# Kernel tuning notes

Hardware: AMD Instinct MI355X
Metric: run time of the kernel (lower is better)

Reference implementation:

```python
import jax, jax.numpy as jnp
import numpy as np

B, L, D = 4, 2048, 512
H = 8
DK = 512 // H  # 64
DV = 512 // H  # 64
TEMP = float(np.power(DK, 0.5))
LN_EPS = 1e-5


def setup_inputs() -> dict:
    key = jax.random.key(0)
    ks = jax.random.split(key, 12)
    s = 0.02
    return {
        "q": jax.random.normal(ks[0], (B, L, D), jnp.float32),
        "k": jax.random.normal(ks[1], (B, L, D), jnp.float32),
        "v": jax.random.normal(ks[2], (B, L, D), jnp.float32),
        "mask": jax.random.randint(ks[3], (B, L, L), 0, 2, jnp.int32),
        "wq_w": jax.random.normal(ks[4], (H * DK, D), jnp.float32) * s,
        "wq_b": jnp.zeros((H * DK,), jnp.float32),
        "wv_w": jax.random.normal(ks[5], (H * DV, D), jnp.float32) * s,
        "wv_b": jnp.zeros((H * DV,), jnp.float32),
        "fc_w": jax.random.normal(ks[6], (D, H * DV), jnp.float32) * s,
        "fc_b": jnp.zeros((D,), jnp.float32),
        "ln_g": jnp.ones((D,), jnp.float32),
        "ln_b": jnp.zeros((D,), jnp.float32),
    }


def reference(q, k, v, mask, wq_w, wq_b, wv_w, wv_b, fc_w, fc_b, ln_g, ln_b):
    residual = q
    # NOTE: source module projects k with w_qs (bug preserved faithfully)
    qh = (q @ wq_w.T + wq_b).reshape(B, L, H, DK).transpose(0, 2, 1, 3)  # bhld
    kh = (k @ wq_w.T + wq_b).reshape(B, L, H, DK).transpose(0, 2, 1, 3)
    vh = (v @ wv_w.T + wv_b).reshape(B, L, H, DV).transpose(0, 2, 1, 3)
    attn = jnp.einsum("bhqd,bhkd->bhqk", qh / TEMP, kh)
    attn = jnp.where(mask[:, None, :, :] == 1, -1e9, attn)
    attn = jax.nn.softmax(attn, axis=-1)
    out = jnp.einsum("bhqk,bhkd->bhqd", attn, vh)  # (B, H, L, DV)
    # faithful buffer reinterpretation: .view(n_head, sz_b, L, DV)
    out = out.reshape(H, B, L, DV).transpose(0, 2, 1, 3).reshape(B, L, H * DV)
    out = out @ fc_w.T + fc_b
    x = out + residual
    mu = jnp.mean(x, axis=-1, keepdims=True)
    var = jnp.mean(jnp.square(x - mu), axis=-1, keepdims=True)
    y = (x - mu) / jnp.sqrt(var + LN_EPS) * ln_g + ln_b
    return (y, attn)
```

## Files before the change

### kernel.cpp

```cpp
#include <hip/hip_runtime.h>

#define NB 4
#define NL 2048
#define ND 512
#define NH 8
#define NTOK (NB * NL)

constexpr float LN_EPS = 1e-5f;

typedef __attribute__((ext_vector_type(8))) short bf16x8;
typedef __attribute__((ext_vector_type(4))) float f32x4;

static __device__ __forceinline__ unsigned short f2bf(float f) {
  unsigned u = __builtin_bit_cast(unsigned, f);
  unsigned r = (u + 0x7fffu + ((u >> 16) & 1u)) >> 16;
  return (unsigned short)r;
}

#define GEMM_CORE(X, W)                                                        \
  __shared__ float As[16][64];                                                 \
  __shared__ float Bs[16][64];                                                 \
  const int tid = threadIdx.x;                                                 \
  const int tx = tid & 15, ty = tid >> 4;                                      \
  const int m0 = blockIdx.x * 64, n0 = blockIdx.y * 64;                        \
  const int lrow = tid >> 2, lseg = tid & 3;                                   \
  float acc[4][4] = {};                                                        \
  for (int k0 = 0; k0 < 512; k0 += 16) {                                       \
    const float4 xa = *(const float4*)&X[(size_t)(m0 + lrow) * ND + k0 + lseg * 4]; \
    const float4 wb = *(const float4*)&W[(size_t)(n0 + lrow) * ND + k0 + lseg * 4]; \
    __syncthreads();                                                           \
    As[lseg * 4 + 0][lrow] = xa.x;                                             \
    As[lseg * 4 + 1][lrow] = xa.y;                                             \
    As[lseg * 4 + 2][lrow] = xa.z;                                             \
    As[lseg * 4 + 3][lrow] = xa.w;                                             \
    Bs[lseg * 4 + 0][lrow] = wb.x;                                             \
    Bs[lseg * 4 + 1][lrow] = wb.y;                                             \
    Bs[lseg * 4 + 2][lrow] = wb.z;                                             \
    Bs[lseg * 4 + 3][lrow] = wb.w;                                             \
    __syncthreads();                                                           \
    _Pragma("unroll") for (int kk = 0; kk < 16; ++kk) {                        \
      float av[4], bv[4];                                                      \
      {                                                                        \
        const float4 t = *(const float4*)&As[kk][ty * 4];                      \
        av[0] = t.x; av[1] = t.y; av[2] = t.z; av[3] = t.w;                    \
      }                                                                        \
      {                                                                        \
        const float4 t = *(const float4*)&Bs[kk][tx * 4];                      \
        bv[0] = t.x; bv[1] = t.y; bv[2] = t.z; bv[3] = t.w;                    \
      }                                                                        \
      _Pragma("unroll") for (int i = 0; i < 4; ++i)                            \
      _Pragma("unroll") for (int j = 0; j < 4; ++j)                            \
        acc[i][j] += av[i] * bv[j];                                            \
    }                                                                          \
  }

__global__ __launch_bounds__(256) void gemm_qk_bf16(const float* __restrict__ X,
                                                    const float* __restrict__ W,
                                                    const float* __restrict__ bias,
                                                    unsigned short* __restrict__ out,
                                                    float scale) {
  GEMM_CORE(X, W)
  const int oc = n0 + tx * 4;
  const int hh = n0 >> 6;
#pragma unroll
  for (int i = 0; i < 4; ++i) {
    const int n = m0 + ty * 4 + i;
    const int bb = n >> 11, l = n & 2047;
    ushort4 o;
    o.x = f2bf((acc[i][0] + bias[oc + 0]) * scale);
    o.y = f2bf((acc[i][1] + bias[oc + 1]) * scale);
    o.z = f2bf((acc[i][2] + bias[oc + 2]) * scale);
    o.w = f2bf((acc[i][3] + bias[oc + 3]) * scale);
    *(ushort4*)&out[(((size_t)bb * NH + hh) * NL + l) * 64 + tx * 4] = o;
  }
}

__global__ __launch_bounds__(256) void gemm_v_bf16t(const float* __restrict__ X,
                                                    const float* __restrict__ W,
                                                    const float* __restrict__ bias,
                                                    unsigned short* __restrict__ outT) {
  GEMM_CORE(X, W)
  const int oc = n0 + tx * 4;
  const int hh = n0 >> 6;
  const int n_base = m0 + ty * 4;
  const int bb = n_base >> 11;
  const int l0 = n_base & 2047;
#pragma unroll
  for (int j = 0; j < 4; ++j) {
    const int d = tx * 4 + j;
    ushort4 o;
    o.x = f2bf(acc[0][j] + bias[oc + j]);
    o.y = f2bf(acc[1][j] + bias[oc + j]);
    o.z = f2bf(acc[2][j] + bias[oc + j]);
    o.w = f2bf(acc[3][j] + bias[oc + j]);
    *(ushort4*)&outT[(((size_t)bb * NH + hh) * 64 + d) * NL + l0] = o;
  }
}

__global__ __launch_bounds__(256) void attn_mfma(const unsigned short* __restrict__ qh,
                                                 const unsigned short* __restrict__ kh,
                                                 const unsigned short* __restrict__ vT,
                                                 const int* __restrict__ mask,
                                                 float* __restrict__ attn,
                                                 float* __restrict__ ao) {
  const int b = blockIdx.z, h = blockIdx.y, q0 = blockIdx.x * 64;
  const int bh = b * NH + h;
  __shared__ unsigned short Ks[64 * 72];
  __shared__ unsigned short Vt[64 * 72];
  __shared__ unsigned short Ps[4 * 16 * 72];
  const int tid = threadIdx.x;
  const int w = tid >> 6, lane = tid & 63;
  const int quad = lane >> 4, l15 = lane & 15;

  const size_t qoff = ((size_t)bh * NL + q0 + w * 16 + l15) * 64 + quad * 8;
  const bf16x8 aq0 = *(const bf16x8*)(qh + qoff);
  const bf16x8 aq1 = *(const bf16x8*)(qh + qoff + 32);

  const int srow = tid >> 2;
  const int scol = (tid & 3) * 16;

  float rinv[4] = {0.f, 0.f, 0.f, 0.f};
  unsigned int mbits[16];
#pragma unroll
  for (int i = 0; i < 16; ++i) mbits[i] = 0;

  for (int kt = 0; kt < 32; ++kt) {
    const unsigned short* kg = kh + ((size_t)bh * NL + kt * 64 + srow) * 64 + scol;
    const uint4 k0 = *(const uint4*)kg;
    const uint4 k1 = *(const uint4*)(kg + 8);
    __syncthreads();
    *(uint4*)&Ks[srow * 72 + scol] = k0;
    *(uint4*)&Ks[srow * 72 + scol + 8] = k1;
    __syncthreads();
    f32x4 s[4];
#pragma unroll
    for (int nt = 0; nt < 4; ++nt) {
      const bf16x8 b0 = *(const bf16x8*)&Ks[(nt * 16 + l15) * 72 + quad * 8];
      const bf16x8 b1 = *(const bf16x8*)&Ks[(nt * 16 + l15) * 72 + 32 + quad * 8];
      f32x4 acc = {0.f, 0.f, 0.f, 0.f};
      acc = __builtin_amdgcn_mfma_f32_16x16x32_bf16(aq0, b0, acc, 0, 0, 0);
      acc = __builtin_amdgcn_mfma_f32_16x16x32_bf16(aq1, b1, acc, 0, 0, 0);
      s[nt] = acc;
    }
    unsigned int mb = 0;
#pragma unroll
    for (int r = 0; r < 4; ++r) {
      const size_t mrow = ((size_t)b * NL + q0 + w * 16 + quad * 4 + r) * NL + kt * 64;
#pragma unroll
      for (int nt = 0; nt < 4; ++nt) {
        const int mz = mask[mrow + nt * 16 + l15];
        float e = __expf(s[nt][r]);
        if (mz == 1) {
          mb |= (1u << (nt * 4 + r));
          e = 0.f;
        }
        rinv[r] += e;
      }
    }
    mbits[kt >> 1] |= mb << ((kt & 1) * 16);
  }
#pragma unroll
  for (int r = 0; r < 4; ++r) {
    float v = rinv[r];
    v += __shfl_xor(v, 1);
    v += __shfl_xor(v, 2);
    v += __shfl_xor(v, 4);
    v += __shfl_xor(v, 8);
    rinv[r] = 1.0f / v;
  }

  f32x4 oacc[4];
#pragma unroll
  for (int nt = 0; nt < 4; ++nt) oacc[nt] = (f32x4){0.f, 0.f, 0.f, 0.f};

  for (int kt = 0; kt < 32; ++kt) {
    const unsigned short* kg = kh + ((size_t)bh * NL + kt * 64 + srow) * 64 + scol;
    const unsigned short* vg = vT + ((size_t)bh * 64 + srow) * NL + kt * 64 + scol;
    const uint4 k0 = *(const uint4*)kg;
    const uint4 k1 = *(const uint4*)(kg + 8);
    const uint4 v0 = *(const uint4*)vg;
    const uint4 v1 = *(const uint4*)(vg + 8);
    __syncthreads();
    *(uint4*)&Ks[srow * 72 + scol] = k0;
    *(uint4*)&Ks[srow * 72 + scol + 8] = k1;
    *(uint4*)&Vt[srow * 72 + scol] = v0;
    *(uint4*)&Vt[srow * 72 + scol + 8] = v1;
    __syncthreads();
    f32x4 s[4];
#pragma unroll
    for (int nt = 0; nt < 4; ++nt) {
      const bf16x8 b0 = *(const bf16x8*)&Ks[(nt * 16 + l15) * 72 + quad * 8];
      const bf16x8 b1 = *(const bf16x8*)&Ks[(nt * 16 + l15) * 72 + 32 + quad * 8];
      f32x4 acc = {0.f, 0.f, 0.f, 0.f};
      acc = __builtin_amdgcn_mfma_f32_16x16x32_bf16(aq0, b0, acc, 0, 0, 0);
      acc = __builtin_amdgcn_mfma_f32_16x16x32_bf16(aq1, b1, acc, 0, 0, 0);
      s[nt] = acc;
    }
    const unsigned int mb = mbits[kt >> 1] >> ((kt & 1) * 16);
#pragma unroll
    for (int r = 0; r < 4; ++r) {
      const int q = q0 + w * 16 + quad * 4 + r;
      float* arow = attn + ((size_t)bh * NL + q) * NL + kt * 64;
      unsigned short* prow = &Ps[(w * 16 + quad * 4 + r) * 72];
#pragma unroll
      for (int nt = 0; nt < 4; ++nt) {
        float e = ((mb >> (nt * 4 + r)) & 1u) ? 0.f : __expf(s[nt][r]) * rinv[r];
        arow[nt * 16 + l15] = e;
        prow[nt * 16 + l15] = f2bf(e);
      }
    }
    const bf16x8 pa0 = *(const bf16x8*)&Ps[(w * 16 + l15) * 72 + quad * 8];
    const bf16x8 pa1 = *(const bf16x8*)&Ps[(w * 16 + l15) * 72 + 32 + quad * 8];
#pragma unroll
    for (int nt = 0; nt < 4; ++nt) {
      const bf16x8 vb0 = *(const bf16x8*)&Vt[(nt * 16 + l15) * 72 + quad * 8];
      const bf16x8 vb1 = *(const bf16x8*)&Vt[(nt * 16 + l15) * 72 + 32 + quad * 8];
      oacc[nt] = __builtin_amdgcn_mfma_f32_16x16x32_bf16(pa0, vb0, oacc[nt], 0, 0, 0);
      oacc[nt] = __builtin_amdgcn_mfma_f32_16x16x32_bf16(pa1, vb1, oacc[nt], 0, 0, 0);
    }
  }
#pragma unroll
  for (int r = 0; r < 4; ++r) {
    float* orow = ao + ((size_t)bh * NL + q0 + w * 16 + quad * 4 + r) * 64;
#pragma unroll
    for (int nt = 0; nt < 4; ++nt) orow[nt * 16 + l15] = oacc[nt][r];
  }
}

__global__ __launch_bounds__(256) void fc_gather(const float* __restrict__ AO,
                                                 const float* __restrict__ W,
                                                 const float* __restrict__ bias,
                                                 const float* __restrict__ resid,
                                                 float* __restrict__ Xout) {
  __shared__ float As[16][64];
  __shared__ float Bs[16][64];
  const int tid = threadIdx.x;
  const int tx = tid & 15, ty = tid >> 4;
  const int m0 = blockIdx.x * 64, n0 = blockIdx.y * 64;
  const int lrow = tid >> 2, lseg = tid & 3;
  const int n = m0 + lrow;
  const int b_out = n >> 11;
  const int l_out = n & 2047;
  const int h2 = b_out * 2 + (l_out >> 10);
  const int q2base = (l_out & 1023) << 1;
  float acc[4][4] = {};
  for (int k0 = 0; k0 < 512; k0 += 16) {
    const int c = k0 + lseg * 4;
    const int q2 = q2base | ((c >> 8) & 1);
    const int b2 = (c >> 6) & 3;
    const int d2 = c & 63;
    const float4 xa = *(const float4*)&AO[((size_t)(h2 * 4 + b2) * NL + q2) * 64 + d2];
    const float4 wb = *(const float4*)&W[(size_t)(n0 + lrow) * ND + c];
    __syncthreads();
    As[lseg * 4 + 0][lrow] = xa.x;
    As[lseg * 4 + 1][lrow] = xa.y;
    As[lseg * 4 + 2][lrow] = xa.z;
    As[lseg * 4 + 3][lrow] = xa.w;
    Bs[lseg * 4 + 0][lrow] = wb.x;
    Bs[lseg * 4 + 1][lrow] = wb.y;
    Bs[lseg * 4 + 2][lrow] = wb.z;
    Bs[lseg * 4 + 3][lrow] = wb.w;
    __syncthreads();
#pragma unroll
    for (int kk = 0; kk < 16; ++kk) {
      float av[4], bv[4];
      {
        const float4 t = *(const float4*)&As[kk][ty * 4];
        av[0] = t.x; av[1] = t.y; av[2] = t.z; av[3] = t.w;
      }
      {
        const float4 t = *(const float4*)&Bs[kk][tx * 4];
        bv[0] = t.x; bv[1] = t.y; bv[2] = t.z; bv[3] = t.w;
      }
#pragma unroll
      for (int i = 0; i < 4; ++i)
#pragma unroll
        for (int j = 0; j < 4; ++j) acc[i][j] += av[i] * bv[j];
    }
  }
  const int oc = n0 + tx * 4;
#pragma unroll
  for (int i = 0; i < 4; ++i) {
    const float4 r = *(const float4*)&resid[(size_t)(m0 + ty * 4 + i) * ND + oc];
    float4 o;
    o.x = acc[i][0] + bias[oc + 0] + r.x;
    o.y = acc[i][1] + bias[oc + 1] + r.y;
    o.z = acc[i][2] + bias[oc + 2] + r.z;
    o.w = acc[i][3] + bias[oc + 3] + r.w;
    *(float4*)&Xout[(size_t)(m0 + ty * 4 + i) * ND + oc] = o;
  }
}

__global__ __launch_bounds__(64) void layernorm_k(const float* __restrict__ x,
                                                  const float* __restrict__ g,
                                                  const float* __restrict__ bta,
                                                  float* __restrict__ y) {
  const int n = blockIdx.x;
  const int lane = threadIdx.x;
  const float* row = x + (size_t)n * ND;
  const float4 a = *(const float4*)&row[lane * 8];
  const float4 c = *(const float4*)&row[lane * 8 + 4];
  float s = a.x + a.y + a.z + a.w + c.x + c.y + c.z + c.w;
  float sq = a.x * a.x + a.y * a.y + a.z * a.z + a.w * a.w +
             c.x * c.x + c.y * c.y + c.z * c.z + c.w * c.w;
#pragma unroll
  for (int off = 32; off; off >>= 1) {
    s += __shfl_down(s, off);
    sq += __shfl_down(sq, off);
  }
  s = __shfl(s, 0);
  sq = __shfl(sq, 0);
  const float mu = s * (1.f / 512.f);
  const float var = sq * (1.f / 512.f) - mu * mu;
  const float rstd = rsqrtf(var + LN_EPS);
  float* yo = y + (size_t)n * ND;
  const int c0 = lane * 8;
  float4 o1, o2;
  o1.x = (a.x - mu) * rstd * g[c0 + 0] + bta[c0 + 0];
  o1.y = (a.y - mu) * rstd * g[c0 + 1] + bta[c0 + 1];
  o1.z = (a.z - mu) * rstd * g[c0 + 2] + bta[c0 + 2];
  o1.w = (a.w - mu) * rstd * g[c0 + 3] + bta[c0 + 3];
  o2.x = (c.x - mu) * rstd * g[c0 + 4] + bta[c0 + 4];
  o2.y = (c.y - mu) * rstd * g[c0 + 5] + bta[c0 + 5];
  o2.z = (c.z - mu) * rstd * g[c0 + 6] + bta[c0 + 6];
  o2.w = (c.w - mu) * rstd * g[c0 + 7] + bta[c0 + 7];
  *(float4*)&yo[c0] = o1;
  *(float4*)&yo[c0 + 4] = o2;
}

extern "C" void kernel_launch(void* const* d_in, const int* in_sizes, int n_in,
                              void* d_out, int out_size, void* d_ws, size_t ws_size,
                              hipStream_t stream) {
  const float* q = (const float*)d_in[0];
  const float* k = (const float*)d_in[1];
  const float* v = (const float*)d_in[2];
  const int* mask = (const int*)d_in[3];
  const float* wq_w = (const float*)d_in[4];
  const float* wq_b = (const float*)d_in[5];
  const float* wv_w = (const float*)d_in[6];
  const float* wv_b = (const float*)d_in[7];
  const float* fc_w = (const float*)d_in[8];
  const float* fc_b = (const float*)d_in[9];
  const float* ln_g = (const float*)d_in[10];
  const float* ln_b = (const float*)d_in[11];

  float* y = (float*)d_out;
  float* attn = y + (size_t)NTOK * ND;

  const size_t SZ = (size_t)NTOK * ND;
  unsigned short* qhb = (unsigned short*)d_ws;
  unsigned short* khb = qhb + SZ;
  unsigned short* vTb = khb + SZ;
  float* ao = (float*)(vTb + SZ);
  float* xx = ao + SZ;

  const dim3 gproj(NTOK / 64, ND / 64);
  gemm_qk_bf16<<<gproj, 256, 0, stream>>>(q, wq_w, wq_b, qhb, 0.125f);
  gemm_qk_bf16<<<gproj, 256, 0, stream>>>(k, wq_w, wq_b, khb, 1.0f);
  gemm_v_bf16t<<<gproj, 256, 0, stream>>>(v, wv_w, wv_b, vTb);
  attn_mfma<<<dim3(NL / 64, NH, NB), 256, 0, stream>>>(qhb, khb, vTb, mask, attn, ao);
  fc_gather<<<gproj, 256, 0, stream>>>(ao, fc_w, fc_b, q, xx);
  layernorm_k<<<NTOK, 64, 0, stream>>>(xx, ln_g, ln_b, y);
}
```

Baseline: 0.9995 ms.

## Replace fp32 SIMT projection and output GEMMs with bf16 MFMA kernels

The Q/K/V projection GEMMs and the gathered output-projection GEMM now convert fp32 tiles to bf16 in shared memory and use 16x16x32 bf16 MFMA instructions instead of scalar fp32 FMAs. Each k-step now covers 64 elements instead of 16. The Q/K and transposed-V outputs are staged through shared memory so global stores are coalesced and wide. The aim is to cut the compute cost of the dense projections, at the price of bf16 rounding of the inputs, including the fc input that was previously kept in fp32.

```diff
diff --git a/kernel.cpp b/kernel.cpp
--- a/kernel.cpp
+++ b/kernel.cpp
@@ -17,84 +17,104 @@
   return (unsigned short)r;
 }
 
-#define GEMM_CORE(X, W)                                                        \
-  __shared__ float As[16][64];                                                 \
-  __shared__ float Bs[16][64];                                                 \
+static __device__ __forceinline__ uint2 pk4(const float4 f) {
+  uint2 r;
+  r.x = (unsigned)f2bf(f.x) | ((unsigned)f2bf(f.y) << 16);
+  r.y = (unsigned)f2bf(f.z) | ((unsigned)f2bf(f.w) << 16);
+  return r;
+}
+
+#define MFMA_GEMM_PRELUDE                                                      \
+  __shared__ unsigned short As[64 * 72];                                       \
+  __shared__ unsigned short Bs[64 * 72];                                       \
   const int tid = threadIdx.x;                                                 \
-  const int tx = tid & 15, ty = tid >> 4;                                      \
+  const int w = tid >> 6;                                                      \
+  const int lane = tid & 63;                                                   \
+  const int quad = lane >> 4, l15 = lane & 15;                                 \
   const int m0 = blockIdx.x * 64, n0 = blockIdx.y * 64;                        \
-  const int lrow = tid >> 2, lseg = tid & 3;                                   \
-  float acc[4][4] = {};                                                        \
-  for (int k0 = 0; k0 < 512; k0 += 16) {                                       \
-    const float4 xa = *(const float4*)&X[(size_t)(m0 + lrow) * ND + k0 + lseg * 4]; \
-    const float4 wb = *(const float4*)&W[(size_t)(n0 + lrow) * ND + k0 + lseg * 4]; \
+  const int srow = tid >> 2;                                                   \
+  const int c4 = (tid & 3) * 4;                                                \
+  const int scol = (tid & 3) * 16;                                             \
+  f32x4 acc[4];                                                                \
+  acc[0] = acc[1] = acc[2] = acc[3] = (f32x4){0.f, 0.f, 0.f, 0.f};
+
+#define MFMA_STEP(AV, BV)                                                      \
+  do {                                                                         \
     __syncthreads();                                                           \
-    As[lseg * 4 + 0][lrow] = xa.x;                                             \
-    As[lseg * 4 + 1][lrow] = xa.y;                                             \
-    As[lseg * 4 + 2][lrow] = xa.z;                                             \
-    As[lseg * 4 + 3][lrow] = xa.w;                                             \
-    Bs[lseg * 4 + 0][lrow] = wb.x;                                             \
-    Bs[lseg * 4 + 1][lrow] = wb.y;                                             \
-    Bs[lseg * 4 + 2][lrow] = wb.z;                                             \
-    Bs[lseg * 4 + 3][lrow] = wb.w;                                             \
+    _Pragma("unroll") for (int j = 0; j < 4; ++j) {                            \
+      *(uint2*)&As[srow * 72 + c4 + j * 16] = pk4(AV[j]);                      \
+      *(uint2*)&Bs[srow * 72 + c4 + j * 16] = pk4(BV[j]);                      \
+    }                                                                          \
     __syncthreads();                                                           \
-    _Pragma("unroll") for (int kk = 0; kk < 16; ++kk) {                        \
-      float av[4], bv[4];                                                      \
-      {                                                                        \
-        const float4 t = *(const float4*)&As[kk][ty * 4];                      \
-        av[0] = t.x; av[1] = t.y; av[2] = t.z; av[3] = t.w;                    \
+    _Pragma("unroll") for (int ks = 0; ks < 2; ++ks) {                         \
+      const bf16x8 af = *(const bf16x8*)&As[(w * 16 + l15) * 72 + ks * 32 + quad * 8]; \
+      _Pragma("unroll") for (int nt = 0; nt < 4; ++nt) {                       \
+        const bf16x8 bfr = *(const bf16x8*)&Bs[(nt * 16 + l15) * 72 + ks * 32 + quad * 8]; \
+        acc[nt] = __builtin_amdgcn_mfma_f32_16x16x32_bf16(af, bfr, acc[nt], 0, 0, 0); \
       }                                                                        \
-      {                                                                        \
-        const float4 t = *(const float4*)&Bs[kk][tx * 4];                      \
-        bv[0] = t.x; bv[1] = t.y; bv[2] = t.z; bv[3] = t.w;                    \
-      }                                                                        \
-      _Pragma("unroll") for (int i = 0; i < 4; ++i)                            \
-      _Pragma("unroll") for (int j = 0; j < 4; ++j)                            \
-        acc[i][j] += av[i] * bv[j];                                            \
     }                                                                          \
-  }
-
-__global__ __launch_bounds__(256) void gemm_qk_bf16(const float* __restrict__ X,
+  } while (0)
+
+__global__ __launch_bounds__(256) void gemm_qk_mfma(const float* __restrict__ X,
                                                     const float* __restrict__ W,
                                                     const float* __restrict__ bias,
                                                     unsigned short* __restrict__ out,
                                                     float scale) {
-  GEMM_CORE(X, W)
-  const int oc = n0 + tx * 4;
+  MFMA_GEMM_PRELUDE
+  for (int k0 = 0; k0 < 512; k0 += 64) {
+    float4 av[4], bv[4];
+#pragma unroll
+    for (int j = 0; j < 4; ++j) {
+      av[j] = *(const float4*)&X[(size_t)(m0 + srow) * ND + k0 + c4 + j * 16];
+      bv[j] = *(const float4*)&W[(size_t)(n0 + srow) * ND + k0 + c4 + j * 16];
+    }
+    MFMA_STEP(av, bv);
+  }
   const int hh = n0 >> 6;
-#pragma unroll
-  for (int i = 0; i < 4; ++i) {
-    const int n = m0 + ty * 4 + i;
-    const int bb = n >> 11, l = n & 2047;
-    ushort4 o;
-    o.x = f2bf((acc[i][0] + bias[oc + 0]) * scale);
-    o.y = f2bf((acc[i][1] + bias[oc + 1]) * scale);
-    o.z = f2bf((acc[i][2] + bias[oc + 2]) * scale);
-    o.w = f2bf((acc[i][3] + bias[oc + 3]) * scale);
-    *(ushort4*)&out[(((size_t)bb * NH + hh) * NL + l) * 64 + tx * 4] = o;
-  }
-}
-
-__global__ __launch_bounds__(256) void gemm_v_bf16t(const float* __restrict__ X,
-                                                    const float* __restrict__ W,
-                                                    const float* __restrict__ bias,
-                                                    unsigned short* __restrict__ outT) {
-  GEMM_CORE(X, W)
-  const int oc = n0 + tx * 4;
+  __syncthreads();
+#pragma unroll
+  for (int nt = 0; nt < 4; ++nt) {
+    const float b = bias[n0 + nt * 16 + l15];
+#pragma unroll
+    for (int r = 0; r < 4; ++r)
+      As[(w * 16 + quad * 4 + r) * 72 + nt * 16 + l15] = f2bf((acc[nt][r] + b) * scale);
+  }
+  __syncthreads();
+  const int tok = m0 + srow;
+  const int bb = tok >> 11, l = tok & 2047;
+  unsigned short* orow = out + (((size_t)bb * NH + hh) * NL + l) * 64;
+  *(uint4*)&orow[scol] = *(const uint4*)&As[srow * 72 + scol];
+  *(uint4*)&orow[scol + 8] = *(const uint4*)&As[srow * 72 + scol + 8];
+}
+
+__global__ __launch_bounds__(256) void gemm_v_mfma_t(const float* __restrict__ X,
+                                                     const float* __restrict__ W,
+                                                     const float* __restrict__ bias,
+                                                     unsigned short* __restrict__ outT) {
+  MFMA_GEMM_PRELUDE
+  for (int k0 = 0; k0 < 512; k0 += 64) {
+    float4 av[4], bv[4];
+#pragma unroll
+    for (int j = 0; j < 4; ++j) {
+      av[j] = *(const float4*)&X[(size_t)(m0 + srow) * ND + k0 + c4 + j * 16];
+      bv[j] = *(const float4*)&W[(size_t)(n0 + srow) * ND + k0 + c4 + j * 16];
+    }
+    MFMA_STEP(av, bv);
+  }
   const int hh = n0 >> 6;
-  const int n_base = m0 + ty * 4;
-  const int bb = n_base >> 11;
-  const int l0 = n_base & 2047;
-#pragma unroll
-  for (int j = 0; j < 4; ++j) {
-    const int d = tx * 4 + j;
-    ushort4 o;
-    o.x = f2bf(acc[0][j] + bias[oc + j]);
-    o.y = f2bf(acc[1][j] + bias[oc + j]);
-    o.z = f2bf(acc[2][j] + bias[oc + j]);
-    o.w = f2bf(acc[3][j] + bias[oc + j]);
-    *(ushort4*)&outT[(((size_t)bb * NH + hh) * 64 + d) * NL + l0] = o;
-  }
+  __syncthreads();
+#pragma unroll
+  for (int nt = 0; nt < 4; ++nt) {
+    const float b = bias[n0 + nt * 16 + l15];
+#pragma unroll
+    for (int r = 0; r < 4; ++r)
+      As[(nt * 16 + l15) * 72 + w * 16 + quad * 4 + r] = f2bf(acc[nt][r] + b);
+  }
+  __syncthreads();
+  const int bb = m0 >> 11, l0 = m0 & 2047;
+  unsigned short* orow = outT + (((size_t)bb * NH + hh) * 64 + srow) * NL + l0;
+  *(uint4*)&orow[scol] = *(const uint4*)&As[srow * 72 + scol];
+  *(uint4*)&orow[scol + 8] = *(const uint4*)&As[srow * 72 + scol + 8];
 }
 
 __global__ __launch_bounds__(256) void attn_mfma(const unsigned short* __restrict__ qh,
@@ -227,67 +247,38 @@
   }
 }
 
-__global__ __launch_bounds__(256) void fc_gather(const float* __restrict__ AO,
-                                                 const float* __restrict__ W,
-                                                 const float* __restrict__ bias,
-                                                 const float* __restrict__ resid,
-                                                 float* __restrict__ Xout) {
-  __shared__ float As[16][64];
-  __shared__ float Bs[16][64];
-  const int tid = threadIdx.x;
-  const int tx = tid & 15, ty = tid >> 4;
-  const int m0 = blockIdx.x * 64, n0 = blockIdx.y * 64;
-  const int lrow = tid >> 2, lseg = tid & 3;
-  const int n = m0 + lrow;
-  const int b_out = n >> 11;
-  const int l_out = n & 2047;
+__global__ __launch_bounds__(256) void fc_gather_mfma(const float* __restrict__ AO,
+                                                      const float* __restrict__ W,
+                                                      const float* __restrict__ bias,
+                                                      const float* __restrict__ resid,
+                                                      float* __restrict__ Xout) {
+  MFMA_GEMM_PRELUDE
+  const int nrow = m0 + srow;
+  const int b_out = nrow >> 11;
+  const int l_out = nrow & 2047;
   const int h2 = b_out * 2 + (l_out >> 10);
   const int q2base = (l_out & 1023) << 1;
-  float acc[4][4] = {};
-  for (int k0 = 0; k0 < 512; k0 += 16) {
-    const int c = k0 + lseg * 4;
-    const int q2 = q2base | ((c >> 8) & 1);
-    const int b2 = (c >> 6) & 3;
-    const int d2 = c & 63;
-    const float4 xa = *(const float4*)&AO[((size_t)(h2 * 4 + b2) * NL + q2) * 64 + d2];
-    const float4 wb = *(const float4*)&W[(size_t)(n0 + lrow) * ND + c];
-    __syncthreads();
-    As[lseg * 4 + 0][lrow] = xa.x;
-    As[lseg * 4 + 1][lrow] = xa.y;
-    As[lseg * 4 + 2][lrow] = xa.z;
-    As[lseg * 4 + 3][lrow] = xa.w;
-    Bs[lseg * 4 + 0][lrow] = wb.x;
-    Bs[lseg * 4 + 1][lrow] = wb.y;
-    Bs[lseg * 4 + 2][lrow] = wb.z;
-    Bs[lseg * 4 + 3][lrow] = wb.w;
-    __syncthreads();
-#pragma unroll
-    for (int kk = 0; kk < 16; ++kk) {
-      float av[4], bv[4];
-      {
-        const float4 t = *(const float4*)&As[kk][ty * 4];
-        av[0] = t.x; av[1] = t.y; av[2] = t.z; av[3] = t.w;
-      }
-      {
-        const float4 t = *(const float4*)&Bs[kk][tx * 4];
-        bv[0] = t.x; bv[1] = t.y; bv[2] = t.z; bv[3] = t.w;
-      }
-#pragma unroll
-      for (int i = 0; i < 4; ++i)
-#pragma unroll
-        for (int j = 0; j < 4; ++j) acc[i][j] += av[i] * bv[j];
-    }
-  }
-  const int oc = n0 + tx * 4;
-#pragma unroll
-  for (int i = 0; i < 4; ++i) {
-    const float4 r = *(const float4*)&resid[(size_t)(m0 + ty * 4 + i) * ND + oc];
-    float4 o;
-    o.x = acc[i][0] + bias[oc + 0] + r.x;
-    o.y = acc[i][1] + bias[oc + 1] + r.y;
-    o.z = acc[i][2] + bias[oc + 2] + r.z;
-    o.w = acc[i][3] + bias[oc + 3] + r.w;
-    *(float4*)&Xout[(size_t)(m0 + ty * 4 + i) * ND + oc] = o;
+  for (int k0 = 0; k0 < 512; k0 += 64) {
+    const int q2 = q2base | ((k0 >> 8) & 1);
+    const int b2 = (k0 >> 6) & 3;
+    const float* abase = AO + ((size_t)(h2 * 4 + b2) * NL + q2) * 64;
+    float4 av[4], bv[4];
+#pragma unroll
+    for (int j = 0; j < 4; ++j) {
+      av[j] = *(const float4*)&abase[c4 + j * 16];
+      bv[j] = *(const float4*)&W[(size_t)(n0 + srow) * ND + k0 + c4 + j * 16];
+    }
+    MFMA_STEP(av, bv);
+  }
+#pragma unroll
+  for (int nt = 0; nt < 4; ++nt) {
+    const float b = bias[n0 + nt * 16 + l15];
+#pragma unroll
+    for (int r = 0; r < 4; ++r) {
+      const int row = m0 + w * 16 + quad * 4 + r;
+      const float rv = resid[(size_t)row * ND + n0 + nt * 16 + l15];
+      Xout[(size_t)row * ND + n0 + nt * 16 + l15] = acc[nt][r] + b + rv;
+    }
   }
 }
 
@@ -355,10 +346,10 @@
   float* xx = ao + SZ;
 
   const dim3 gproj(NTOK / 64, ND / 64);
-  gemm_qk_bf16<<<gproj, 256, 0, stream>>>(q, wq_w, wq_b, qhb, 0.125f);
-  gemm_qk_bf16<<<gproj, 256, 0, stream>>>(k, wq_w, wq_b, khb, 1.0f);
-  gemm_v_bf16t<<<gproj, 256, 0, stream>>>(v, wv_w, wv_b, vTb);
+  gemm_qk_mfma<<<gproj, 256, 0, stream>>>(q, wq_w, wq_b, qhb, 0.125f);
+  gemm_qk_mfma<<<gproj, 256, 0, stream>>>(k, wq_w, wq_b, khb, 1.0f);
+  gemm_v_mfma_t<<<gproj, 256, 0, stream>>>(v, wv_w, wv_b, vTb);
   attn_mfma<<<dim3(NL / 64, NH, NB), 256, 0, stream>>>(qhb, khb, vTb, mask, attn, ao);
-  fc_gather<<<gproj, 256, 0, stream>>>(ao, fc_w, fc_b, q, xx);
+  fc_gather_mfma<<<gproj, 256, 0, stream>>>(ao, fc_w, fc_b, q, xx);
   layernorm_k<<<NTOK, 64, 0, stream>>>(xx, ln_g, ln_b, y);
 }
```

Result: faster. 870.4 us (-12.9%).
